# Kernel tuning notes

Measured on AMD Instinct MI355X. Metric: run time of the kernel, lower is better.

## Reference

```python
import jax, jax.numpy as jnp
import numpy as np

K = 8        # k nearest neighbors (module init arg)
HEADS = 8


def setup_inputs() -> dict:
    key = jax.random.key(0)
    ks = jax.random.split(key, 5)
    B, N, D = 2, 4096, 512
    x = jax.random.normal(ks[0], (B, N, D), dtype=jnp.float32)
    coords = jax.random.uniform(ks[1], (B, N, 2), dtype=jnp.float32) * 100.0
    w_qkv = jax.random.normal(ks[2], (3 * D, D), dtype=jnp.float32) * 0.02
    w_proj = jax.random.normal(ks[3], (D, D), dtype=jnp.float32) * 0.02
    b_proj = jax.random.normal(ks[4], (D,), dtype=jnp.float32) * 0.02
    return {"x": x, "coords": coords, "w_qkv": w_qkv, "w_proj": w_proj, "b_proj": b_proj}


def reference(x, coords, w_qkv, w_proj, b_proj):
    B, N, D = x.shape
    H = HEADS
    hd = D // H
    k_actual = min(K + 1, N)

    # pairwise euclidean distances (B, N, N), as torch.cdist
    d2 = (jnp.sum(coords**2, -1)[:, :, None]
          + jnp.sum(coords**2, -1)[:, None, :]
          - 2.0 * jnp.einsum('bnc,bmc->bnm', coords, coords))
    dist = jnp.sqrt(jnp.maximum(d2, 0.0))

    # k-NN indices: topk of -dist  -> (B, N, k_actual)
    _, nn_idx = jax.lax.top_k(-dist, k_actual)

    # gather neighbor features: (B, N, k, D)
    x_nb = jax.vmap(lambda xb, ib: xb[ib])(x, nn_idx)

    # qkv projections (Linear, no bias): y = x @ W^T
    qkv_c = jnp.einsum('bnd,ed->bne', x, w_qkv)          # (B, N, 3D)
    q = qkv_c[..., :D].reshape(B, N, H, hd)              # (B, N, H, hd)
    qkv_n = jnp.einsum('bnkd,ed->bnke', x_nb, w_qkv)     # (B, N, k, 3D)
    k_n = qkv_n[..., D:2 * D].reshape(B, N, k_actual, H, hd)
    v_n = qkv_n[..., 2 * D:].reshape(B, N, k_actual, H, hd)

    # attention over k neighbors
    attn = jnp.einsum('bnhd,bnkhd->bnhk', q, k_n) / jnp.sqrt(jnp.float32(hd))
    attn = jax.nn.softmax(attn, axis=-1)
    out = jnp.einsum('bnhk,bnkhd->bnhd', attn, v_n).reshape(B, N, D)

    # proj(GELU(out)) with exact (erf) GELU as nn.GELU default
    out = jax.nn.gelu(out, approximate=False)
    out = jnp.einsum('bnd,ed->bne', out, w_proj) + b_proj
    return x + out
```

## Files before the change

kernel.cpp:

```cpp
#include <hip/hip_runtime.h>
#include <hip/hip_bf16.h>

using bf16 = __hip_bfloat16;

typedef __attribute__((ext_vector_type(8))) __bf16 bf16x8;
typedef __attribute__((ext_vector_type(4))) float f32x4;

#define NPTS 4096
#define DMODEL 512
#define HDIM 64
#define KNN 9
#define MROWS 8192

#define GRIDW 32
#define CELLW 3.125f
#define NCELL (GRIDW * GRIDW)

#define NN_BYTES    (MROWS * 16 * 4)
#define QKV_BYTES   ((size_t)MROWS * 1536 * 2)
#define G_BYTES     ((size_t)MROWS * 512 * 2)
#define XB_BYTES    ((size_t)MROWS * 512 * 2)
#define WQ_BYTES    ((size_t)1536 * 512 * 2)
#define WP_BYTES    ((size_t)512 * 512 * 2)
#define GSTART_BYTES (2 * 1025 * 4)
#define SXY_BYTES    ((size_t)2 * NPTS * 8)
#define SIDX_BYTES   ((size_t)2 * NPTS * 4)

__global__ __launch_bounds__(256) void cvt_kernel(
    const float4* __restrict__ s0, ushort4* __restrict__ d0, int n0,
    const float4* __restrict__ s1, ushort4* __restrict__ d1, int n1,
    const float4* __restrict__ s2, ushort4* __restrict__ d2, int n2) {
    int g = blockIdx.x * 256 + threadIdx.x;
    const float4* s; ushort4* d; int i;
    if (g < n0) { s = s0; d = d0; i = g; }
    else if (g < n0 + n1) { s = s1; d = d1; i = g - n0; }
    else if (g < n0 + n1 + n2) { s = s2; d = d2; i = g - n0 - n1; }
    else return;
    float4 v = s[i];
    bf16 b0 = __float2bfloat16(v.x), b1 = __float2bfloat16(v.y);
    bf16 b2 = __float2bfloat16(v.z), b3 = __float2bfloat16(v.w);
    ushort4 o;
    o.x = *reinterpret_cast<unsigned short*>(&b0);
    o.y = *reinterpret_cast<unsigned short*>(&b1);
    o.z = *reinterpret_cast<unsigned short*>(&b2);
    o.w = *reinterpret_cast<unsigned short*>(&b3);
    d[i] = o;
}

__global__ __launch_bounds__(1024) void grid_build(const float* __restrict__ coords,
                                                   int* __restrict__ gstart,
                                                   float2* __restrict__ sxy,
                                                   int* __restrict__ sidx) {
    __shared__ int cnt[NCELL];
    __shared__ int off2[NCELL];
    __shared__ int sstart[NCELL];
    __shared__ int wsum[16];
    const int b = blockIdx.x, tid = threadIdx.x;
    cnt[tid] = 0; off2[tid] = 0;
    __syncthreads();
    const float2* c2 = (const float2*)(coords + (size_t)b * NPTS * 2);
    float px[4], py[4]; int pc[4];
#pragma unroll
    for (int i = 0; i < 4; ++i) {
        int p = tid + i * 1024;
        float2 v = c2[p];
        px[i] = v.x; py[i] = v.y;
        int cx = min(GRIDW - 1, (int)(v.x / CELLW));
        int cy = min(GRIDW - 1, (int)(v.y / CELLW));
        pc[i] = cy * GRIDW + cx;
        atomicAdd(&cnt[pc[i]], 1);
    }
    __syncthreads();
    const int v = cnt[tid];
    const int lane = tid & 63, wv = tid >> 6;
    int inc = v;
#pragma unroll
    for (int o = 1; o < 64; o <<= 1) {
        int t = __shfl_up(inc, o, 64);
        if (lane >= o) inc += t;
    }
    if (lane == 63) wsum[wv] = inc;
    __syncthreads();
    if (tid < 16) {
        int w = wsum[tid];
#pragma unroll
        for (int o = 1; o < 16; o <<= 1) {
            int t = __shfl_up(w, o, 16);
            if (tid >= o) w += t;
        }
        wsum[tid] = w;
    }
    __syncthreads();
    const int excl = inc - v + (wv ? wsum[wv - 1] : 0);
    sstart[tid] = excl;
    gstart[b * 1025 + tid] = excl;
    if (tid == 1023) gstart[b * 1025 + 1024] = excl + v;
    __syncthreads();
#pragma unroll
    for (int i = 0; i < 4; ++i) {
        int o = atomicAdd(&off2[pc[i]], 1);
        int pos = sstart[pc[i]] + o;
        sxy[(size_t)b * NPTS + pos]  = make_float2(px[i], py[i]);
        sidx[(size_t)b * NPTS + pos] = tid + i * 1024;
    }
}

__global__ __launch_bounds__(256) void knn_grid(const float* __restrict__ coords,
                                                const int* __restrict__ gstart,
                                                const float2* __restrict__ sxy,
                                                const int* __restrict__ sidx,
                                                int* __restrict__ nn_out) {
    const int wv = threadIdx.x >> 6, lane = threadIdx.x & 63;
    const int q = blockIdx.x * 4 + wv;
    const int b = q >> 12, n = q & 4095;
    const float2* cb = (const float2*)(coords + (size_t)b * NPTS * 2);
    const float2 pq = cb[n];
    const float xn = pq.x, yn = pq.y;
    const float sn = __fadd_rn(__fmul_rn(xn, xn), __fmul_rn(yn, yn));
    const int cx = min(GRIDW - 1, (int)(xn / CELLW));
    const int cy = min(GRIDW - 1, (int)(yn / CELLW));
    const int* gs = gstart + b * 1025;
    const float2* xy = sxy + (size_t)b * NPTS;
    const int* id = sidx + (size_t)b * NPTS;

    float d9 = 0.0f;
    int outi[9];
    for (int r = 2;; ++r) {
        float bd[10]; int bi[10];
#pragma unroll
        for (int j = 0; j < 10; ++j) { bd[j] = 3.4e38f; bi[j] = 0x7fffffff; }
        const int ylo = max(cy - r, 0), yhi = min(cy + r, GRIDW - 1);
        const int xlo = max(cx - r, 0), xhi = min(cx + r, GRIDW - 1);
        for (int ry = ylo; ry <= yhi; ++ry) {
            const int s0 = gs[ry * GRIDW + xlo];
            const int s1 = gs[ry * GRIDW + xhi + 1];
            for (int p0 = s0; p0 < s1; p0 += 64) {
                const int pp = p0 + lane;
                float d = 3.4e38f; int idx = 0x7fffffff;
                if (pp < s1) {
                    float2 cm = xy[pp];
                    idx = id[pp];
                    float sc  = __fadd_rn(__fmul_rn(cm.x, cm.x), __fmul_rn(cm.y, cm.y));
                    float dot = __fadd_rn(__fmul_rn(xn, cm.x), __fmul_rn(yn, cm.y));
                    float d2  = __fsub_rn(__fadd_rn(sn, sc), __fmul_rn(2.0f, dot));
                    d = sqrtf(fmaxf(d2, 0.0f));
                }
                if (d < bd[8]) {
#pragma unroll
                    for (int j = 8; j >= 1; --j) {
                        if (d < bd[j]) {
                            bool t2 = d < bd[j - 1];
                            bd[j] = t2 ? bd[j - 1] : d;
                            bi[j] = t2 ? bi[j - 1] : idx;
                        }
                    }
                    if (d < bd[0]) { bd[0] = d; bi[0] = idx; }
                }
            }
        }
        unsigned long long head =
            ((unsigned long long)__float_as_uint(bd[0]) << 32) | (unsigned)bi[0];
#pragma unroll
        for (int rr = 0; rr < 9; ++rr) {
            unsigned long long m = head;
#pragma unroll
            for (int s2 = 32; s2 > 0; s2 >>= 1) {
                unsigned long long o = __shfl_xor(m, s2, 64);
                m = o < m ? o : m;
            }
            outi[rr] = (int)(unsigned)(m & 0xffffffffULL);
            if (rr == 8) d9 = __uint_as_float((unsigned)(m >> 32));
            if (m == head) {
#pragma unroll
                for (int j = 0; j < 9; ++j) { bd[j] = bd[j + 1]; bi[j] = bi[j + 1]; }
                head = ((unsigned long long)__float_as_uint(bd[0]) << 32) | (unsigned)bi[0];
            }
        }
        if (d9 <= (float)r * CELLW - 0.01f || r >= 34) break;
    }
    if (lane == 0) {
        int* o = nn_out + (size_t)q * 16;
#pragma unroll
        for (int rr = 0; rr < 9; ++rr) o[rr] = outi[rr];
    }
}

__device__ __forceinline__ void gload16(const bf16* g, bf16* l) {
    __builtin_amdgcn_global_load_lds(
        (const __attribute__((address_space(1))) unsigned int*)g,
        (__attribute__((address_space(3))) unsigned int*)l,
        16, 0, 0);
}

template <bool EPI>
__global__ __launch_bounds__(256) void gemm_bt(const bf16* __restrict__ A,
                                               const bf16* __restrict__ W,
                                               void* __restrict__ Cout,
                                               int Nn, int Kd,
                                               const float* __restrict__ bias,
                                               const float* __restrict__ resid) {
    __shared__ __attribute__((aligned(16))) bf16 As[2][128][32];
    __shared__ __attribute__((aligned(16))) bf16 Bs[2][128][32];

    const int tid = threadIdx.x;
    const int rowBase = blockIdx.x * 128;
    const int colBase = blockIdx.y * 128;
    const int nk = Kd >> 5;

    const int lane = tid & 63, w = tid >> 6;
    const int wr = w >> 1, wc = w & 1;

    const int r0  = tid >> 2;
    const int kk0 = (tid & 3) * 8;

    f32x4 acc[4][4] = {};

    const bf16* gaBase = A + (size_t)(rowBase + r0) * Kd + kk0;
    const bf16* gbBase = W + (size_t)(colBase + r0) * Kd + kk0;

#define STAGE(bufi, kt)                                                     \
    do {                                                                    \
        const bf16* ga = gaBase + (size_t)(kt) * 32;                        \
        const bf16* gb = gbBase + (size_t)(kt) * 32;                        \
        gload16(ga,                   &As[bufi][r0][kk0]);                  \
        gload16(ga + (size_t)64 * Kd, &As[bufi][r0 + 64][kk0]);             \
        gload16(gb,                   &Bs[bufi][r0][kk0]);                  \
        gload16(gb + (size_t)64 * Kd, &Bs[bufi][r0 + 64][kk0]);             \
    } while (0)

    STAGE(0, 0);
    __syncthreads();

    int buf = 0;
    const int r16 = lane & 15;
    const int hk  = (lane >> 4) * 8;
    for (int kt = 0; kt < nk; ++kt) {
        if (kt + 1 < nk) STAGE(buf ^ 1, kt + 1);

        bf16x8 afr[4], bfr[4];
#pragma unroll
        for (int m2 = 0; m2 < 4; ++m2)
            afr[m2] = *(const bf16x8*)&As[buf][wr * 64 + m2 * 16 + r16][hk];
#pragma unroll
        for (int n2 = 0; n2 < 4; ++n2)
            bfr[n2] = *(const bf16x8*)&Bs[buf][wc * 64 + n2 * 16 + r16][hk];
#pragma unroll
        for (int m2 = 0; m2 < 4; ++m2)
#pragma unroll
            for (int n2 = 0; n2 < 4; ++n2)
                acc[m2][n2] = __builtin_amdgcn_mfma_f32_16x16x32_bf16(
                    afr[m2], bfr[n2], acc[m2][n2], 0, 0, 0);

        __syncthreads();
        buf ^= 1;
    }
#undef STAGE

    const int r4  = (lane >> 4) * 4;
    const int c16 = lane & 15;
#pragma unroll
    for (int m2 = 0; m2 < 4; ++m2) {
#pragma unroll
        for (int n2 = 0; n2 < 4; ++n2) {
            const int gc = colBase + wc * 64 + n2 * 16 + c16;
#pragma unroll
            for (int r = 0; r < 4; ++r) {
                const int gr = rowBase + wr * 64 + m2 * 16 + r4 + r;
                float v = acc[m2][n2][r];
                if (EPI) {
                    v = v + bias[gc];
                    v = resid[(size_t)gr * Nn + gc] + v;
                    ((float*)Cout)[(size_t)gr * Nn + gc] = v;
                } else {
                    ((bf16*)Cout)[(size_t)gr * Nn + gc] = __float2bfloat16(v);
                }
            }
        }
    }
}

__global__ __launch_bounds__(256) void attn_kernel(const bf16* __restrict__ qkv,
                                                   const int* __restrict__ nn,
                                                   bf16* __restrict__ g) {
    const int wv = threadIdx.x >> 6, lane = threadIdx.x & 63;
    const int q = blockIdx.x * 4 + wv;
    const int b = q >> 12;
    const int rowbase = b * NPTS;

    const int* nnq = nn + (size_t)q * 16;
    int idxs[KNN];
#pragma unroll
    for (int j = 0; j < KNN; ++j) idxs[j] = nnq[j];

    bf16x8 qv = *(const bf16x8*)(qkv + (size_t)q * 1536 + lane * 8);
    float qf[8];
#pragma unroll
    for (int e = 0; e < 8; ++e) qf[e] = (float)qv[e];

    float lg[KNN];
#pragma unroll
    for (int j = 0; j < KNN; ++j) {
        const bf16x8 kv = *(const bf16x8*)(
            qkv + (size_t)(rowbase + idxs[j]) * 1536 + DMODEL + lane * 8);
        float p = 0.0f;
#pragma unroll
        for (int e = 0; e < 8; ++e) p += qf[e] * (float)kv[e];
        p += __shfl_xor(p, 1, 64);
        p += __shfl_xor(p, 2, 64);
        p += __shfl_xor(p, 4, 64);
        lg[j] = p * 0.125f;
    }
    float mx = lg[0];
#pragma unroll
    for (int j = 1; j < KNN; ++j) mx = fmaxf(mx, lg[j]);
    float wgt[KNN], ssum = 0.0f;
#pragma unroll
    for (int j = 0; j < KNN; ++j) { wgt[j] = expf(lg[j] - mx); ssum += wgt[j]; }
    const float inv = 1.0f / ssum;

    float o[8] = {};
#pragma unroll
    for (int j = 0; j < KNN; ++j) {
        const bf16x8 vv = *(const bf16x8*)(
            qkv + (size_t)(rowbase + idxs[j]) * 1536 + 2 * DMODEL + lane * 8);
        const float wj = wgt[j] * inv;
#pragma unroll
        for (int e = 0; e < 8; ++e) o[e] += wj * (float)vv[e];
    }
    bf16x8 ov;
#pragma unroll
    for (int e = 0; e < 8; ++e) {
        float ge = 0.5f * o[e] * (1.0f + erff(o[e] * 0.70710678118654752f));
        ov[e] = (__bf16)__float2bfloat16(ge);
    }
    *(bf16x8*)(g + (size_t)q * DMODEL + lane * 8) = ov;
}

extern "C" void kernel_launch(void* const* d_in, const int* in_sizes, int n_in,
                              void* d_out, int out_size, void* d_ws, size_t ws_size,
                              hipStream_t stream) {
    const float* x      = (const float*)d_in[0];
    const float* coords = (const float*)d_in[1];
    const float* w_qkv  = (const float*)d_in[2];
    const float* w_proj = (const float*)d_in[3];
    const float* b_proj = (const float*)d_in[4];
    float* out = (float*)d_out;

    char* wsb = (char*)d_ws;
    size_t off = 0;
    int*    nn     = (int*)(wsb + off);    off += NN_BYTES;
    bf16*   qkv    = (bf16*)(wsb + off);   off += QKV_BYTES;
    bf16*   g      = (bf16*)(wsb + off);   off += G_BYTES;
    bf16*   xb     = (bf16*)(wsb + off);   off += XB_BYTES;
    bf16*   wqb    = (bf16*)(wsb + off);   off += WQ_BYTES;
    bf16*   wpb    = (bf16*)(wsb + off);   off += WP_BYTES;
    int*    gstart = (int*)(wsb + off);    off += GSTART_BYTES;
    float2* sxy    = (float2*)(wsb + off); off += SXY_BYTES;
    int*    sidx   = (int*)(wsb + off);    off += SIDX_BYTES;

    const int n0 = 4194304 / 4, n1 = 786432 / 4, n2 = 262144 / 4;
    const int ntot = n0 + n1 + n2;
    cvt_kernel<<<(ntot + 255) / 256, 256, 0, stream>>>(
        (const float4*)x, (ushort4*)xb, n0,
        (const float4*)w_qkv, (ushort4*)wqb, n1,
        (const float4*)w_proj, (ushort4*)wpb, n2);

    grid_build<<<2, 1024, 0, stream>>>(coords, gstart, sxy, sidx);
    knn_grid<<<2048, 256, 0, stream>>>(coords, gstart, sxy, sidx, nn);
    gemm_bt<false><<<dim3(64, 12), 256, 0, stream>>>(xb, wqb, qkv, 1536, 512,
                                                     nullptr, nullptr);
    attn_kernel<<<2048, 256, 0, stream>>>(qkv, nn, g);
    gemm_bt<true><<<dim3(64, 4), 256, 0, stream>>>(g, wpb, out, 512, 512,
                                                   b_proj, x);
}
```

Before: 153.9 us.

## Merge independent kernels into shared launches to overlap kNN with GEMM

The bf16 conversion and the spatial grid build now run in one launch, with the block index choosing the role. The QKV GEMM and the kNN search likewise share one launch, so their blocks can run concurrently on different CUs. The aim is to cut launch gaps and let latency-bound kNN work overlap compute-bound GEMM work. The cost is shared-memory and register allocation sized for the heavier role in each merged kernel, which may lower occupancy for the kNN blocks.

```diff
diff --git a/kernel.cpp b/kernel.cpp
--- a/kernel.cpp
+++ b/kernel.cpp
@@ -26,36 +26,38 @@
 #define SXY_BYTES    ((size_t)2 * NPTS * 8)
 #define SIDX_BYTES   ((size_t)2 * NPTS * 4)
 
-__global__ __launch_bounds__(256) void cvt_kernel(
+__global__ __launch_bounds__(1024) void prep_kernel(
     const float4* __restrict__ s0, ushort4* __restrict__ d0, int n0,
     const float4* __restrict__ s1, ushort4* __restrict__ d1, int n1,
-    const float4* __restrict__ s2, ushort4* __restrict__ d2, int n2) {
-    int g = blockIdx.x * 256 + threadIdx.x;
-    const float4* s; ushort4* d; int i;
-    if (g < n0) { s = s0; d = d0; i = g; }
-    else if (g < n0 + n1) { s = s1; d = d1; i = g - n0; }
-    else if (g < n0 + n1 + n2) { s = s2; d = d2; i = g - n0 - n1; }
-    else return;
-    float4 v = s[i];
-    bf16 b0 = __float2bfloat16(v.x), b1 = __float2bfloat16(v.y);
-    bf16 b2 = __float2bfloat16(v.z), b3 = __float2bfloat16(v.w);
-    ushort4 o;
-    o.x = *reinterpret_cast<unsigned short*>(&b0);
-    o.y = *reinterpret_cast<unsigned short*>(&b1);
-    o.z = *reinterpret_cast<unsigned short*>(&b2);
-    o.w = *reinterpret_cast<unsigned short*>(&b3);
-    d[i] = o;
-}
-
-__global__ __launch_bounds__(1024) void grid_build(const float* __restrict__ coords,
-                                                   int* __restrict__ gstart,
-                                                   float2* __restrict__ sxy,
-                                                   int* __restrict__ sidx) {
+    const float4* __restrict__ s2, ushort4* __restrict__ d2, int n2,
+    const float* __restrict__ coords,
+    int* __restrict__ gstart,
+    float2* __restrict__ sxy,
+    int* __restrict__ sidx) {
     __shared__ int cnt[NCELL];
     __shared__ int off2[NCELL];
     __shared__ int sstart[NCELL];
     __shared__ int wsum[16];
-    const int b = blockIdx.x, tid = threadIdx.x;
+
+    if (blockIdx.x < 1280) {
+        int g = blockIdx.x * 1024 + threadIdx.x;
+        const float4* s; ushort4* d; int i;
+        if (g < n0) { s = s0; d = d0; i = g; }
+        else if (g < n0 + n1) { s = s1; d = d1; i = g - n0; }
+        else { s = s2; d = d2; i = g - n0 - n1; }
+        float4 v = s[i];
+        bf16 b0 = __float2bfloat16(v.x), b1 = __float2bfloat16(v.y);
+        bf16 b2 = __float2bfloat16(v.z), b3 = __float2bfloat16(v.w);
+        ushort4 o;
+        o.x = *reinterpret_cast<unsigned short*>(&b0);
+        o.y = *reinterpret_cast<unsigned short*>(&b1);
+        o.z = *reinterpret_cast<unsigned short*>(&b2);
+        o.w = *reinterpret_cast<unsigned short*>(&b3);
+        d[i] = o;
+        return;
+    }
+
+    const int b = blockIdx.x - 1280, tid = threadIdx.x;
     cnt[tid] = 0; off2[tid] = 0;
     __syncthreads();
     const float2* c2 = (const float2*)(coords + (size_t)b * NPTS * 2);
@@ -105,13 +107,93 @@
     }
 }
 
-__global__ __launch_bounds__(256) void knn_grid(const float* __restrict__ coords,
-                                                const int* __restrict__ gstart,
-                                                const float2* __restrict__ sxy,
-                                                const int* __restrict__ sidx,
-                                                int* __restrict__ nn_out) {
-    const int wv = threadIdx.x >> 6, lane = threadIdx.x & 63;
-    const int q = blockIdx.x * 4 + wv;
+__device__ __forceinline__ void gload16(const bf16* g, bf16* l) {
+    __builtin_amdgcn_global_load_lds(
+        (const __attribute__((address_space(1))) unsigned int*)g,
+        (__attribute__((address_space(3))) unsigned int*)l,
+        16, 0, 0);
+}
+
+__global__ __launch_bounds__(256) void mid_kernel(
+    const bf16* __restrict__ A, const bf16* __restrict__ W,
+    bf16* __restrict__ Cout,
+    const float* __restrict__ coords, const int* __restrict__ gstart,
+    const float2* __restrict__ sxy, const int* __restrict__ sidx,
+    int* __restrict__ nn_out) {
+    __shared__ __attribute__((aligned(16))) bf16 As[2][128][32];
+    __shared__ __attribute__((aligned(16))) bf16 Bs[2][128][32];
+
+    const int tid = threadIdx.x;
+    const int lane = tid & 63;
+
+    if (blockIdx.x < 768) {
+        const int Nn = 1536, Kd = 512, nk = 16;
+        const int rowBase = (blockIdx.x & 63) * 128;
+        const int colBase = (blockIdx.x >> 6) * 128;
+        const int w = tid >> 6;
+        const int wr = w >> 1, wc = w & 1;
+        const int r0  = tid >> 2;
+        const int kk0 = (tid & 3) * 8;
+
+        f32x4 acc[4][4] = {};
+        const bf16* gaBase = A + (size_t)(rowBase + r0) * Kd + kk0;
+        const bf16* gbBase = W + (size_t)(colBase + r0) * Kd + kk0;
+
+#define STAGE(bufi, kt)                                                     \
+        do {                                                                \
+            const bf16* ga = gaBase + (size_t)(kt) * 32;                    \
+            const bf16* gb = gbBase + (size_t)(kt) * 32;                    \
+            gload16(ga,                   &As[bufi][r0][kk0]);              \
+            gload16(ga + (size_t)64 * Kd, &As[bufi][r0 + 64][kk0]);         \
+            gload16(gb,                   &Bs[bufi][r0][kk0]);              \
+            gload16(gb + (size_t)64 * Kd, &Bs[bufi][r0 + 64][kk0]);         \
+        } while (0)
+
+        STAGE(0, 0);
+        __syncthreads();
+
+        int buf = 0;
+        const int r16 = lane & 15;
+        const int hk  = (lane >> 4) * 8;
+        for (int kt = 0; kt < nk; ++kt) {
+            if (kt + 1 < nk) STAGE(buf ^ 1, kt + 1);
+            bf16x8 afr[4], bfr[4];
+#pragma unroll
+            for (int m2 = 0; m2 < 4; ++m2)
+                afr[m2] = *(const bf16x8*)&As[buf][wr * 64 + m2 * 16 + r16][hk];
+#pragma unroll
+            for (int n2 = 0; n2 < 4; ++n2)
+                bfr[n2] = *(const bf16x8*)&Bs[buf][wc * 64 + n2 * 16 + r16][hk];
+#pragma unroll
+            for (int m2 = 0; m2 < 4; ++m2)
+#pragma unroll
+                for (int n2 = 0; n2 < 4; ++n2)
+                    acc[m2][n2] = __builtin_amdgcn_mfma_f32_16x16x32_bf16(
+                        afr[m2], bfr[n2], acc[m2][n2], 0, 0, 0);
+            __syncthreads();
+            buf ^= 1;
+        }
+#undef STAGE
+
+        const int r4  = (lane >> 4) * 4;
+        const int c16 = lane & 15;
+#pragma unroll
+        for (int m2 = 0; m2 < 4; ++m2) {
+#pragma unroll
+            for (int n2 = 0; n2 < 4; ++n2) {
+                const int gc = colBase + wc * 64 + n2 * 16 + c16;
+#pragma unroll
+                for (int r = 0; r < 4; ++r) {
+                    const int gr = rowBase + wr * 64 + m2 * 16 + r4 + r;
+                    Cout[(size_t)gr * Nn + gc] = __float2bfloat16(acc[m2][n2][r]);
+                }
+            }
+        }
+        return;
+    }
+
+    const int wv = tid >> 6;
+    const int q = (blockIdx.x - 768) * 4 + wv;
     const int b = q >> 12, n = q & 4095;
     const float2* cb = (const float2*)(coords + (size_t)b * NPTS * 2);
     const float2 pq = cb[n];
@@ -185,36 +267,24 @@
     }
 }
 
-__device__ __forceinline__ void gload16(const bf16* g, bf16* l) {
-    __builtin_amdgcn_global_load_lds(
-        (const __attribute__((address_space(1))) unsigned int*)g,
-        (__attribute__((address_space(3))) unsigned int*)l,
-        16, 0, 0);
-}
-
-template <bool EPI>
-__global__ __launch_bounds__(256) void gemm_bt(const bf16* __restrict__ A,
-                                               const bf16* __restrict__ W,
-                                               void* __restrict__ Cout,
-                                               int Nn, int Kd,
-                                               const float* __restrict__ bias,
-                                               const float* __restrict__ resid) {
+__global__ __launch_bounds__(256) void gemm_epi(const bf16* __restrict__ A,
+                                                const bf16* __restrict__ W,
+                                                float* __restrict__ Cout,
+                                                const float* __restrict__ bias,
+                                                const float* __restrict__ resid) {
     __shared__ __attribute__((aligned(16))) bf16 As[2][128][32];
     __shared__ __attribute__((aligned(16))) bf16 Bs[2][128][32];
 
+    const int Nn = 512, Kd = 512, nk = 16;
     const int tid = threadIdx.x;
     const int rowBase = blockIdx.x * 128;
     const int colBase = blockIdx.y * 128;
-    const int nk = Kd >> 5;
-
     const int lane = tid & 63, w = tid >> 6;
     const int wr = w >> 1, wc = w & 1;
-
     const int r0  = tid >> 2;
     const int kk0 = (tid & 3) * 8;
 
     f32x4 acc[4][4] = {};
-
     const bf16* gaBase = A + (size_t)(rowBase + r0) * Kd + kk0;
     const bf16* gbBase = W + (size_t)(colBase + r0) * Kd + kk0;
 
@@ -236,7 +306,6 @@
     const int hk  = (lane >> 4) * 8;
     for (int kt = 0; kt < nk; ++kt) {
         if (kt + 1 < nk) STAGE(buf ^ 1, kt + 1);
-
         bf16x8 afr[4], bfr[4];
 #pragma unroll
         for (int m2 = 0; m2 < 4; ++m2)
@@ -250,7 +319,6 @@
             for (int n2 = 0; n2 < 4; ++n2)
                 acc[m2][n2] = __builtin_amdgcn_mfma_f32_16x16x32_bf16(
                     afr[m2], bfr[n2], acc[m2][n2], 0, 0, 0);
-
         __syncthreads();
         buf ^= 1;
     }
@@ -266,14 +334,9 @@
 #pragma unroll
             for (int r = 0; r < 4; ++r) {
                 const int gr = rowBase + wr * 64 + m2 * 16 + r4 + r;
-                float v = acc[m2][n2][r];
-                if (EPI) {
-                    v = v + bias[gc];
-                    v = resid[(size_t)gr * Nn + gc] + v;
-                    ((float*)Cout)[(size_t)gr * Nn + gc] = v;
-                } else {
-                    ((bf16*)Cout)[(size_t)gr * Nn + gc] = __float2bfloat16(v);
-                }
+                float v = acc[m2][n2][r] + bias[gc];
+                v = resid[(size_t)gr * Nn + gc] + v;
+                Cout[(size_t)gr * Nn + gc] = v;
             }
         }
     }
@@ -359,17 +422,15 @@
     int*    sidx   = (int*)(wsb + off);    off += SIDX_BYTES;
 
     const int n0 = 4194304 / 4, n1 = 786432 / 4, n2 = 262144 / 4;
-    const int ntot = n0 + n1 + n2;
-    cvt_kernel<<<(ntot + 255) / 256, 256, 0, stream>>>(
+    prep_kernel<<<1282, 1024, 0, stream>>>(
         (const float4*)x, (ushort4*)xb, n0,
         (const float4*)w_qkv, (ushort4*)wqb, n1,
-        (const float4*)w_proj, (ushort4*)wpb, n2);
-
-    grid_build<<<2, 1024, 0, stream>>>(coords, gstart, sxy, sidx);
-    knn_grid<<<2048, 256, 0, stream>>>(coords, gstart, sxy, sidx, nn);
-    gemm_bt<false><<<dim3(64, 12), 256, 0, stream>>>(xb, wqb, qkv, 1536, 512,
-                                                     nullptr, nullptr);
+        (const float4*)w_proj, (ushort4*)wpb, n2,
+        coords, gstart, sxy, sidx);
+
+    mid_kernel<<<2816, 256, 0, stream>>>(xb, wqb, qkv, coords, gstart, sxy,
+                                         sidx, nn);
+
     attn_kernel<<<2048, 256, 0, stream>>>(qkv, nn, g);
-    gemm_bt<true><<<dim3(64, 4), 256, 0, stream>>>(g, wpb, out, 512, 512,
-                                                   b_proj, x);
-}
+    gemm_epi<<<dim3(64, 4), 256, 0, stream>>>(g, wpb, out, b_proj, x);
+}
```

Measured after the change: 161.9 us. 1.05x slower.
